# Kernel tuning notes

Hardware: AMD Instinct MI355X
Metric: run time of the kernel (lower is better)

The kernel has to match this reference:

```python
import jax, jax.numpy as jnp
import numpy as np
from jax import lax

B, CIN, H, W = 16, 64, 128, 128
NUM_CLASSES = 80
K = 100              # cfg.TEST.TOPK
SCORE_THRESH = 0.2   # hardcoded in decode()
NMS_THRESH = 0.5     # cfg.TEST.NMS_THRESH
RATIO = 4.0          # inp_downsample_ratio


def setup_inputs() -> dict:
    key = jax.random.key(0)
    ks = jax.random.split(key, 8)
    def w(k, shape, scale=0.05):
        return jax.random.normal(k, shape, dtype=jnp.float32) * scale
    inp = {"x": jax.random.normal(ks[0], (B, CIN, H, W), dtype=jnp.float32)}
    for i, (name, cout) in enumerate([("cls", NUM_CLASSES), ("reg", 2), ("wh", 2)]):
        inp[f"{name}_w1"] = w(ks[1 + 2 * i], (64, CIN, 3, 3))
        inp[f"{name}_b1"] = jnp.zeros((64,), jnp.float32)
        inp[f"{name}_w2"] = w(ks[2 + 2 * i], (cout, 64, 1, 1))
        # cls 1x1 conv bias filled with -2.19 as in the torch module
        inp[f"{name}_b2"] = jnp.full((cout,), -2.19 if name == "cls" else 0.0, jnp.float32)
    return inp


def _conv(x, w, b):
    y = lax.conv_general_dilated(x, w, (1, 1), 'SAME',
                                 dimension_numbers=('NCHW', 'OIHW', 'NCHW'))
    return y + b[None, :, None, None]


def _branch(x, w1, b1, w2, b2):
    return _conv(jax.nn.relu(_conv(x, w1, b1)), w2, b2)


def _nms_keep(boxes, valid):
    # boxes: [K,4] sorted by score desc (top_k output); valid: [K] bool
    x1, y1, x2, y2 = boxes[:, 0], boxes[:, 1], boxes[:, 2], boxes[:, 3]
    area = (x2 - x1) * (y2 - y1)
    iw = jnp.clip(jnp.minimum(x2[:, None], x2[None, :]) - jnp.maximum(x1[:, None], x1[None, :]), 0.0)
    ih = jnp.clip(jnp.minimum(y2[:, None], y2[None, :]) - jnp.maximum(y1[:, None], y1[None, :]), 0.0)
    inter = iw * ih
    iou = inter / (area[:, None] + area[None, :] - inter + 1e-9)  # [K,K]
    idx = jnp.arange(K)
    def step(keep, i):
        sup = (iou[i] > NMS_THRESH) & (idx > i) & keep[i]
        return keep & ~sup, None
    keep, _ = lax.scan(step, valid, idx)
    return keep


def reference(x, cls_w1, cls_b1, cls_w2, cls_b2,
              reg_w1, reg_b1, reg_w2, reg_b2,
              wh_w1, wh_b1, wh_w2, wh_b2):
    cls = jax.nn.sigmoid(_branch(x, cls_w1, cls_b1, cls_w2, cls_b2))  # [B,C,H,W]
    reg = jax.nn.sigmoid(_branch(x, reg_w1, reg_b1, reg_w2, reg_b2))  # [B,2,H,W]
    wh = jnp.exp(_branch(x, wh_w1, wh_b1, wh_w2, wh_b2))              # [B,2,H,W]

    # 3x3 max-pool peak NMS (torch max_pool2d pads with -inf; SAME matches k=3,s=1,p=1)
    pooled = lax.reduce_window(cls, -jnp.inf, lax.max, (1, 1, 3, 3), (1, 1, 1, 1), 'SAME')
    cls = cls * (pooled == cls).astype(cls.dtype)

    cls_f = cls.transpose(0, 2, 3, 1).reshape(B, H * W, NUM_CLASSES)
    reg_f = reg.transpose(0, 2, 3, 1).reshape(B, H * W, 2)
    wh_f = wh.transpose(0, 2, 3, 1).reshape(B, H * W, 2)

    scores_all = jnp.max(cls_f, axis=-1)              # [B,HW]
    cats_all = jnp.argmax(cls_f, axis=-1)             # [B,HW]
    scores, inds = lax.top_k(scores_all, K)           # [B,K], sorted desc
    valid = scores > SCORE_THRESH                     # fixed-size mask instead of dynamic filter

    cats = jnp.take_along_axis(cats_all, inds, axis=1)
    reg_k = jnp.take_along_axis(reg_f, inds[..., None], axis=1)   # [B,K,2]
    wh_k = jnp.take_along_axis(wh_f, inds[..., None], axis=1)     # [B,K,2]

    gy, gx = jnp.meshgrid(jnp.arange(H), jnp.arange(W), indexing='ij')
    grids = jnp.stack([gx, gy], axis=-1).reshape(-1, 2).astype(jnp.float32)  # [HW,2] (x,y)
    ct = grids[inds] + reg_k                                       # [B,K,2]
    boxes = jnp.concatenate([ct - wh_k / 2.0, ct + wh_k / 2.0], axis=-1) * RATIO  # [B,K,4]

    keep = jax.vmap(_nms_keep)(boxes, valid)          # [B,K] bool
    return boxes, cats, scores, keep
```

## Files before the change

### kernel.cpp

```cpp
#include <hip/hip_runtime.h>
#include <math.h>

#define BN 16
#define HWSZ 16384
#define NC 80
#define KK 100

typedef _Float16 f16;
typedef _Float16 f16x2 __attribute__((ext_vector_type(2)));
typedef _Float16 f16x4 __attribute__((ext_vector_type(4)));
typedef _Float16 f16x8 __attribute__((ext_vector_type(8)));
typedef float    f32x4 __attribute__((ext_vector_type(4)));
typedef unsigned int uint;
typedef unsigned long long u64;

#define WS_CLS   0
#define CLS_SZ   (BN*NC*HWSZ)
#define WS_REG   (WS_CLS + CLS_SZ)
#define REG_SZ   (BN*2*HWSZ)
#define WS_WH    (WS_REG + REG_SZ)
#define WH_SZ    (BN*2*HWSZ)
#define WS_SC    (WS_WH + WH_SZ)
#define SC_SZ    (BN*HWSZ)
#define WS_CAT   (WS_SC + SC_SZ)
#define CAT_SZ   (BN*HWSZ)
#define WS_W1H   (WS_CAT + CAT_SZ)
#define W1F      (110592/2)
#define WS_W1L   (WS_W1H + W1F)
#define WS_W2H   (WS_W1L + W1F)
#define W2F      (7168/2)
#define WS_W2L   (WS_W2H + W2F)
#define NREG     (BN*128*2*2)
#define WS_XTH   (WS_W2L + W2F)
#define XT_F     (NREG*2112/2)
#define WS_XTL   (WS_XTH + XT_F)
#define WS_ZR    (WS_XTL + XT_F)
#define ZR_F     1056
#define WS_SC1   (WS_ZR + ZR_F)
#define WS_CAT1  (WS_SC1 + SC_SZ)
#define WS_SC2   (WS_CAT1 + CAT_SZ)
#define WS_CAT2  (WS_SC2 + SC_SZ)
#define WS_SC3   (WS_CAT2 + CAT_SZ)
#define WS_CAT3  (WS_SC3 + SC_SZ)
#define WS_SC4   (WS_CAT3 + CAT_SZ)
#define WS_CAT4  (WS_SC4 + SC_SZ)
#define WS_SC5   (WS_CAT4 + CAT_SZ)
#define WS_CAT5  (WS_SC5 + SC_SZ)
#define WS_SC6   (WS_CAT5 + CAT_SZ)
#define WS_CAT6  (WS_SC6 + SC_SZ)
#define WS_SC7   (WS_CAT6 + CAT_SZ)
#define WS_CAT7  (WS_SC7 + SC_SZ)
#define WS_END8  (WS_CAT7 + CAT_SZ)

#define SCL_X   16.0f
#define SCL_W   256.0f
#define INV_ACC (1.0f/4096.0f)

#define GL2LDS(g, l) __builtin_amdgcn_global_load_lds( \
    (__attribute__((address_space(1))) unsigned int*)(unsigned long long)(const void*)(g), \
    (__attribute__((address_space(3))) unsigned int*)(unsigned int)(unsigned long long)(void*)(l), \
    16, 0, 0)

__global__ void k_prep(const float* __restrict__ cw1, const float* __restrict__ rw1,
                       const float* __restrict__ ww1, const float* __restrict__ cw2,
                       const float* __restrict__ rw2, const float* __restrict__ ww2,
                       f16* __restrict__ w1h, f16* __restrict__ w1l,
                       f16* __restrict__ w2h, f16* __restrict__ w2l,
                       float* __restrict__ zr) {
    int idx = blockIdx.x * 256 + threadIdx.x;
    if (idx < 3*9*64*64) {
        int ci = idx & 63, co = (idx >> 6) & 63;
        int s  = (idx >> 12) % 9, br = idx / 36864;
        const float* src = (br == 0) ? cw1 : (br == 1 ? rw1 : ww1);
        float v = src[(co*64 + ci)*9 + s] * SCL_W;
        f16 h = (f16)v;
        w1h[idx] = h; w1l[idx] = (f16)(v - (float)h);
    }
    int j = idx - 3*9*64*64;
    if (j >= 0 && j < 112*64) {
        int ci = j & 63, row = j >> 6;
        float v = 0.f;
        if (row < 80)                    v = cw2[row*64 + ci];
        else if (row < 82)               v = rw2[(row-80)*64 + ci];
        else if (row >= 96 && row < 98)  v = ww2[(row-96)*64 + ci];
        v *= SCL_W;
        f16 h = (f16)v;
        w2h[j] = h; w2l[j] = (f16)(v - (float)h);
    }
    if (zr && idx < ZR_F) zr[idx] = 0.f;
}

__global__ __launch_bounds__(256) void k_prepx(const float* __restrict__ x,
                                               f16* __restrict__ xth,
                                               f16* __restrict__ xtl) {
    const int reg = blockIdx.x;
    const int chunk = reg & 1, hh = (reg >> 1) & 1;
    const int gy = (reg >> 2) & 127, b = reg >> 9;
    __shared__ f16 th[66*72] __attribute__((aligned(16)));
    __shared__ f16 tl[66*72] __attribute__((aligned(16)));
    const int tid = threadIdx.x;
    const float* xb = x + ((size_t)(b*64 + chunk*32))*HWSZ + gy*128;
    #pragma unroll
    for (int it = 0; it < 9; it++) {
        int idx = it*256 + tid;
        if (idx < 2112) {
            int ci = idx / 66, pxi = idx - ci*66;
            int gp = hh*64 - 1 + pxi;
            float v = 0.f;
            if (gp >= 0 && gp < 128) v = xb[(size_t)ci*HWSZ + gp] * SCL_X;
            f16 hv = (f16)v;
            th[pxi*72 + ci] = hv;
            tl[pxi*72 + ci] = (f16)(v - (float)hv);
        }
    }
    __syncthreads();
    f16* oh = xth + (size_t)reg*2112;
    f16* ol = xtl + (size_t)reg*2112;
    {
        int row = tid >> 2, q = tid & 3;
        int sq = q ^ ((row >> 1) & 3);
        *(f16x8*)(oh + row*32 + sq*8) = *(const f16x8*)(th + row*72 + q*8);
        *(f16x8*)(ol + row*32 + sq*8) = *(const f16x8*)(tl + row*72 + q*8);
        if (tid < 8) {
            int u2 = 256 + tid, row2 = u2 >> 2, q2 = u2 & 3;
            int sq2 = q2 ^ ((row2 >> 1) & 3);
            *(f16x8*)(oh + row2*32 + sq2*8) = *(const f16x8*)(th + row2*72 + q2*8);
            *(f16x8*)(ol + row2*32 + sq2*8) = *(const f16x8*)(tl + row2*72 + q2*8);
        }
    }
}

#define ABUF 8448
__global__ __launch_bounds__(256, 2) void k_conv(
    const f16* __restrict__ xth, const f16* __restrict__ xtl, const f16* __restrict__ zreg,
    const f16* __restrict__ w1h, const f16* __restrict__ w1l,
    const f16* __restrict__ w2h, const f16* __restrict__ w2l,
    const float* __restrict__ b1c, const float* __restrict__ b1r, const float* __restrict__ b1w,
    const float* __restrict__ b2c, const float* __restrict__ b2r, const float* __restrict__ b2w,
    float* __restrict__ cls_o, float* __restrict__ reg_o, float* __restrict__ wh_o)
{
    __shared__ char smem[7*ABUF] __attribute__((aligned(16)));
    f16* Rh = (f16*)smem;
    f16* Rl = (f16*)(smem + 9216);

    const int p  = blockIdx.x + 2*blockIdx.y + 128*blockIdx.z;
    const int lg = (p & 7)*256 + (p >> 3);
    const int b  = lg >> 7;
    const int y0 = ((lg & 127) >> 1) * 2;
    const int h  = lg & 1;

    const int tid = threadIdx.x;
    const int w = tid >> 6, lane = tid & 63;
    const int l15 = lane & 15, quad = lane >> 4;
    const int co = w*16 + l15;

    #define STAGE1(ch, gyi, bufi) do {                                        \
        const int gy_ = y0 - 1 + (gyi);                                       \
        const f16* sh_; const f16* sl_;                                       \
        if (gy_ >= 0 && gy_ < 128) {                                          \
            size_t ro_ = (size_t)(((b*128 + gy_)*2 + h)*2 + (ch)) * 2112;     \
            sh_ = xth + ro_; sl_ = xtl + ro_;                                 \
        } else { sh_ = zreg; sl_ = zreg; }                                    \
        char* db_ = smem + (bufi)*ABUF;                                       \
        GL2LDS(sh_ + tid*8, db_ + tid*16);                                    \
        GL2LDS(sl_ + tid*8, db_ + 4224 + tid*16);                             \
        if (tid < 8) {                                                        \
            GL2LDS(sh_ + 2048 + tid*8, db_ + 4096 + tid*16);                  \
            GL2LDS(sl_ + 2048 + tid*8, db_ + 4224 + 4096 + tid*16);           \
        }                                                                     \
    } while (0)

    f32x4 accA[3][4], accB[3][4];
    #pragma unroll
    for (int br = 0; br < 3; br++)
        #pragma unroll
        for (int m = 0; m < 4; m++) {
            accA[br][m] = (f32x4){0.f,0.f,0.f,0.f};
            accB[br][m] = (f32x4){0.f,0.f,0.f,0.f};
        }

    #define CSTEP(ph, rr, A0p, A1p) do {                                      \
        const f16* A0 = (const f16*)(A0p);                                    \
        const f16* A1 = (const f16*)(A1p);                                    \
        _Pragma("unroll")                                                     \
        for (int dx = 0; dx < 3; dx++) {                                      \
            const int s = (rr)*3 + dx;                                        \
            f16x8 bh[3], bl[3];                                               \
            _Pragma("unroll")                                                 \
            for (int br = 0; br < 3; br++) {                                  \
                size_t k = ((size_t)((br*9 + s)*64 + co))*64 + (ph)*32 + quad*8; \
                bh[br] = *(const f16x8*)(w1h + k);                            \
                bl[br] = *(const f16x8*)(w1l + k);                            \
            }                                                                 \
            __builtin_amdgcn_s_setprio(1);                                    \
            _Pragma("unroll")                                                 \
            for (int m = 0; m < 4; m++) {                                     \
                const int row = m*16 + l15 + dx;                              \
                const int off = row*32 + ((quad ^ ((row >> 1) & 3)) << 3);    \
                {                                                             \
                    f16x8 ah0 = *(const f16x8*)(A0 + off);                    \
                    f16x8 al0 = *(const f16x8*)(A0 + 2112 + off);             \
                    _Pragma("unroll")                                         \
                    for (int br = 0; br < 3; br++) {                          \
                        accA[br][m] = __builtin_amdgcn_mfma_f32_16x16x32_f16(ah0, bh[br], accA[br][m], 0,0,0); \
                        accA[br][m] = __builtin_amdgcn_mfma_f32_16x16x32_f16(ah0, bl[br], accA[br][m], 0,0,0); \
                        accA[br][m] = __builtin_amdgcn_mfma_f32_16x16x32_f16(al0, bh[br], accA[br][m], 0,0,0); \
                    }                                                         \
                }                                                             \
                {                                                             \
                    f16x8 ah1 = *(const f16x8*)(A1 + off);                    \
                    f16x8 al1 = *(const f16x8*)(A1 + 2112 + off);             \
                    _Pragma("unroll")                                         \
                    for (int br = 0; br < 3; br++) {                          \
                        accB[br][m] = __builtin_amdgcn_mfma_f32_16x16x32_f16(ah1, bh[br], accB[br][m], 0,0,0); \
                        accB[br][m] = __builtin_amdgcn_mfma_f32_16x16x32_f16(ah1, bl[br], accB[br][m], 0,0,0); \
                        accB[br][m] = __builtin_amdgcn_mfma_f32_16x16x32_f16(al1, bh[br], accB[br][m], 0,0,0); \
                    }                                                         \
                }                                                             \
            }                                                                 \
            __builtin_amdgcn_s_setprio(0);                                    \
        }                                                                     \
    } while (0)

    #pragma unroll
    for (int gyi = 0; gyi < 4; gyi++) STAGE1(0, gyi, gyi);
    #pragma unroll
    for (int gyi = 0; gyi < 3; gyi++) STAGE1(1, gyi, 4 + gyi);
    __syncthreads();

    for (int r = 0; r < 3; r++)
        CSTEP(0, r, smem + r*ABUF, smem + (r+1)*ABUF);

    __syncthreads();
    STAGE1(1, 3, 0);

    for (int r = 0; r < 2; r++)
        CSTEP(1, r, smem + (4+r)*ABUF, smem + (5+r)*ABUF);

    __syncthreads();
    CSTEP(1, 2, smem + 6*ABUF, smem + 0*ABUF);

    #undef STAGE1
    #undef CSTEP

    #define EPIROW(ACC, yy) do {                                              \
        __syncthreads();                        \
        _Pragma("unroll")                                                     \
        for (int m = 0; m < 4; m++)                                           \
            _Pragma("unroll")                                                 \
            for (int rg = 0; rg < 4; rg++) {                                  \
                float t = fmaxf(ACC[br][m][rg]*INV_ACC + b1v, 0.f) * SCL_X;   \
                f16 hh = (f16)t;                                              \
                int pxl = m*16 + quad*4 + rg;                                 \
                Rh[pxl*72 + co] = hh;                                         \
                Rl[pxl*72 + co] = (f16)(t - (float)hh);                       \
            }                                                                 \
        __syncthreads();                                                      \
        const int NT     = (br == 0) ? 5 : 1;                                 \
        const int rowoff = (br == 0) ? 0 : (br == 1 ? 80 : 96);               \
        f32x4 a2[5];                                                          \
        _Pragma("unroll")                                                     \
        for (int n = 0; n < 5; n++) a2[n] = (f32x4){0.f,0.f,0.f,0.f};         \
        _Pragma("unroll")                                                     \
        for (int kc = 0; kc < 64; kc += 32) {                                 \
            int off = co*72 + kc + quad*8;                                    \
            f16x8 xh = *(const f16x8*)(Rh + off);                             \
            f16x8 xl = *(const f16x8*)(Rl + off);                             \
            _Pragma("unroll")                                                 \
            for (int n = 0; n < 5; n++) {                                     \
                if (n >= NT) break;                                           \
                const f16* g2h = w2h + (rowoff + n*16 + l15)*64 + kc + quad*8;\
                const f16* g2l = w2l + (rowoff + n*16 + l15)*64 + kc + quad*8;\
                f16x8 bh2 = *(const f16x8*)g2h;                               \
                f16x8 bl2 = *(const f16x8*)g2l;                               \
                a2[n] = __builtin_amdgcn_mfma_f32_16x16x32_f16(xh, bh2, a2[n], 0,0,0); \
                a2[n] = __builtin_amdgcn_mfma_f32_16x16x32_f16(xh, bl2, a2[n], 0,0,0); \
                a2[n] = __builtin_amdgcn_mfma_f32_16x16x32_f16(xl, bh2, a2[n], 0,0,0); \
            }                                                                 \
        }                                                                     \
        const int pxg = h*64 + w*16 + quad*4;                                 \
        if (br == 0) {                                                        \
            _Pragma("unroll")                                                 \
            for (int n = 0; n < 5; n++) {                                     \
                int co2 = n*16 + l15;                                         \
                float bb = b2c[co2];                                          \
                _Pragma("unroll")                                             \
                for (int rg = 0; rg < 4; rg++) {                              \
                    float sv = a2[n][rg]*INV_ACC + bb;                        \
                    cls_o[((size_t)(b*80 + co2)*128 + (yy))*128 + pxg + rg] = 1.f/(1.f + expf(-sv)); \
                }                                                             \
            }                                                                 \
        } else {                                                              \
            if (l15 < 2) {                                                    \
                const float* b2 = (br == 1) ? b2r : b2w;                      \
                float* outp     = (br == 1) ? reg_o : wh_o;                   \
                float bb = b2[l15];                                           \
                _Pragma("unroll")                                             \
                for (int rg = 0; rg < 4; rg++) {                              \
                    float sv = a2[0][rg]*INV_ACC + bb;                        \
                    float o  = (br == 1) ? (1.f/(1.f + expf(-sv))) : expf(sv);\
                    outp[((size_t)(b*2 + l15))*HWSZ + (yy)*128 + pxg + rg] = o; \
                }                                                             \
            }                                                                 \
        }                                                                     \
    } while (0)

    #pragma unroll
    for (int br = 0; br < 3; br++) {
        const float* b1 = (br == 0) ? b1c : (br == 1 ? b1r : b1w);
        const float b1v = b1[co];
        EPIROW(accA, y0);
        EPIROW(accB, y0 + 1);
    }
    #undef EPIROW
}

#define A_STRIDE 36
#define ABUF_FB  9504
__global__ __launch_bounds__(256) void k_conv_fb(
    const float* __restrict__ x,
    const f16* __restrict__ w1h, const f16* __restrict__ w1l,
    const f16* __restrict__ w2h, const f16* __restrict__ w2l,
    const float* __restrict__ b1c, const float* __restrict__ b1r, const float* __restrict__ b1w,
    const float* __restrict__ b2c, const float* __restrict__ b2r, const float* __restrict__ b2w,
    float* __restrict__ cls_o, float* __restrict__ reg_o, float* __restrict__ wh_o)
{
    __shared__ char smem[19008] __attribute__((aligned(16)));
    f16* Rh = (f16*)smem;
    f16* Rl = (f16*)(smem + 9216);

    const int h = blockIdx.x, y = blockIdx.y, b = blockIdx.z;
    const int tid = threadIdx.x;
    const int w = tid >> 6, lane = tid & 63;
    const int l15 = lane & 15, quad = lane >> 4;

    static const int CS[6] = {0,0,0,1,1,1};
    static const int RS[6] = {0,1,2,0,1,2};

    #define STAGEF(bufi, si_) do {                                            \
        const int gy = y - 1 + RS[si_];                                       \
        const bool ok = (gy >= 0) && (gy < 128);                              \
        const float* xp = x + ((size_t)(b*64 + CS[si_]*32)*128 + gy)*128;     \
        f16x2* dh = (f16x2*)(smem + (bufi)*ABUF_FB);                          \
        f16x2* dl = (f16x2*)(smem + (bufi)*ABUF_FB + 4752);                   \
        _Pragma("unroll")                                                     \
        for (int e0 = 0; e0 < 1024; e0 += 256) {                              \
            int e = e0 + tid;                                                 \
            int pxl = e & 63, cp = e >> 6;                                    \
            float v0 = 0.f, v1 = 0.f;                                         \
            if (ok) { int g = h*64 + pxl;                                     \
                      v0 = xp[(size_t)(2*cp)*HWSZ + g]*SCL_X;                 \
                      v1 = xp[(size_t)(2*cp+1)*HWSZ + g]*SCL_X; }             \
            f16 h0 = (f16)v0, h1 = (f16)v1;                                   \
            f16 l0 = (f16)(v0 - (float)h0), l1 = (f16)(v1 - (float)h1);       \
            int wi = (pxl + 1)*18 + cp;                                       \
            dh[wi] = (f16x2){h0, h1};                                         \
            dl[wi] = (f16x2){l0, l1};                                         \
        }                                                                     \
        if (tid < 32) {                                                       \
            int side = tid >> 4, cp = tid & 15;                               \
            bool valid = ok && (side ? (h == 0) : (h == 1));                  \
            int g = side ? 64 : 63;                                           \
            float v0 = 0.f, v1 = 0.f;                                         \
            if (valid) { v0 = xp[(size_t)(2*cp)*HWSZ + g]*SCL_X;              \
                         v1 = xp[(size_t)(2*cp+1)*HWSZ + g]*SCL_X; }          \
            f16 h0 = (f16)v0, h1 = (f16)v1;                                   \
            f16 l0 = (f16)(v0 - (float)h0), l1 = (f16)(v1 - (float)h1);       \
            int wi = (side ? 65 : 0)*18 + cp;                                 \
            dh[wi] = (f16x2){h0, h1};                                         \
            dl[wi] = (f16x2){l0, l1};                                         \
        }                                                                     \
    } while (0)

    f32x4 acc[3][4];
    #pragma unroll
    for (int br = 0; br < 3; br++)
        #pragma unroll
        for (int m = 0; m < 4; m++) acc[br][m] = (f32x4){0.f,0.f,0.f,0.f};

    STAGEF(0, 0);
    __syncthreads();

    for (int si = 0; si < 6; si++) {
        const int cur = si & 1;
        if (si < 5) STAGEF(cur ^ 1, si + 1);
        const f16* APh = (const f16*)(smem + cur*ABUF_FB);
        const f16* APl = APh + 2376;
        const int chunk = CS[si], r = RS[si];
        #pragma unroll
        for (int dx = 0; dx < 3; dx++) {
            const int s = r*3 + dx;
            f16x8 bh[3], bl[3];
            #pragma unroll
            for (int br = 0; br < 3; br++) {
                size_t k = ((size_t)((br*9 + s)*64 + (w*16 + l15)))*64 + chunk*32 + quad*8;
                bh[br] = *(const f16x8*)(w1h + k);
                bl[br] = *(const f16x8*)(w1l + k);
            }
            #pragma unroll
            for (int m = 0; m < 4; m++) {
                int off = (m*16 + l15 + dx)*A_STRIDE + quad*8;
                f16x4 h0 = *(const f16x4*)(APh + off);
                f16x4 h1 = *(const f16x4*)(APh + off + 4);
                f16x4 u0 = *(const f16x4*)(APl + off);
                f16x4 u1 = *(const f16x4*)(APl + off + 4);
                f16x8 ah = __builtin_shufflevector(h0, h1, 0,1,2,3,4,5,6,7);
                f16x8 al = __builtin_shufflevector(u0, u1, 0,1,2,3,4,5,6,7);
                #pragma unroll
                for (int br = 0; br < 3; br++) {
                    acc[br][m] = __builtin_amdgcn_mfma_f32_16x16x32_f16(ah, bh[br], acc[br][m], 0,0,0);
                    acc[br][m] = __builtin_amdgcn_mfma_f32_16x16x32_f16(ah, bl[br], acc[br][m], 0,0,0);
                    acc[br][m] = __builtin_amdgcn_mfma_f32_16x16x32_f16(al, bh[br], acc[br][m], 0,0,0);
                }
            }
        }
        __syncthreads();
    }
    #undef STAGEF

    #pragma unroll
    for (int br = 0; br < 3; br++) {
        const float* b1 = (br == 0) ? b1c : (br == 1 ? b1r : b1w);
        const float b1v = b1[w*16 + l15];
        __syncthreads();
        #pragma unroll
        for (int m = 0; m < 4; m++)
            #pragma unroll
            for (int rg = 0; rg < 4; rg++) {
                float t = fmaxf(acc[br][m][rg]*INV_ACC + b1v, 0.f) * SCL_X;
                f16 hh = (f16)t;
                int pxl = m*16 + quad*4 + rg;
                int co  = w*16 + l15;
                Rh[pxl*72 + co] = hh;
                Rl[pxl*72 + co] = (f16)(t - (float)hh);
            }
        __syncthreads();

        const int NT     = (br == 0) ? 5 : 1;
        const int rowoff = (br == 0) ? 0 : (br == 1 ? 80 : 96);
        f32x4 a2[5];
        #pragma unroll
        for (int n = 0; n < 5; n++) a2[n] = (f32x4){0.f,0.f,0.f,0.f};

        #pragma unroll
        for (int kc = 0; kc < 64; kc += 32) {
            int off = (w*16 + l15)*72 + kc + quad*8;
            f16x8 xh = *(const f16x8*)(Rh + off);
            f16x8 xl = *(const f16x8*)(Rl + off);
            #pragma unroll
            for (int n = 0; n < 5; n++) {
                if (n >= NT) break;
                const f16* g2h = w2h + (rowoff + n*16 + l15)*64 + kc + quad*8;
                const f16* g2l = w2l + (rowoff + n*16 + l15)*64 + kc + quad*8;
                f16x8 bh = *(const f16x8*)g2h;
                f16x8 bl = *(const f16x8*)g2l;
                a2[n] = __builtin_amdgcn_mfma_f32_16x16x32_f16(xh, bh, a2[n], 0,0,0);
                a2[n] = __builtin_amdgcn_mfma_f32_16x16x32_f16(xh, bl, a2[n], 0,0,0);
                a2[n] = __builtin_amdgcn_mfma_f32_16x16x32_f16(xl, bh, a2[n], 0,0,0);
            }
        }

        const int pxg = h*64 + w*16 + quad*4;
        if (br == 0) {
            #pragma unroll
            for (int n = 0; n < 5; n++) {
                int co2 = n*16 + l15;
                float bb = b2c[co2];
                #pragma unroll
                for (int rg = 0; rg < 4; rg++) {
                    float sv = a2[n][rg]*INV_ACC + bb;
                    cls_o[((size_t)(b*80 + co2)*128 + y)*128 + pxg + rg] = 1.f/(1.f + expf(-sv));
                }
            }
        } else {
            if (l15 < 2) {
                const float* b2 = (br == 1) ? b2r : b2w;
                float* outp     = (br == 1) ? reg_o : wh_o;
                float bb = b2[l15];
                #pragma unroll
                for (int rg = 0; rg < 4; rg++) {
                    float sv = a2[0][rg]*INV_ACC + bb;
                    float o  = (br == 1) ? (1.f/(1.f + expf(-sv))) : expf(sv);
                    outp[((size_t)(b*2 + l15))*HWSZ + y*128 + pxg + rg] = o;
                }
            }
        }
    }
}

__global__ __launch_bounds__(256) void k_peaks(const float* __restrict__ cls,
                                               float* __restrict__ s0, int* __restrict__ c0p,
                                               float* __restrict__ s1, int* __restrict__ c1p,
                                               float* __restrict__ s2, int* __restrict__ c2p,
                                               float* __restrict__ s3, int* __restrict__ c3p,
                                               float* __restrict__ s4, int* __restrict__ c4p,
                                               float* __restrict__ s5, int* __restrict__ c5p,
                                               float* __restrict__ s6, int* __restrict__ c6p,
                                               float* __restrict__ s7, int* __restrict__ c7p,
                                               int span) {
    const int b  = blockIdx.y;
    const int z  = blockIdx.z;
    const int c0 = z * span, c1 = c0 + span;
    float* __restrict__ sc  = (z == 0) ? s0 : (z == 1) ? s1 : (z == 2) ? s2 : (z == 3) ? s3
                            : (z == 4) ? s4 : (z == 5) ? s5 : (z == 6) ? s6 : s7;
    int*   __restrict__ cat = (z == 0) ? c0p : (z == 1) ? c1p : (z == 2) ? c2p : (z == 3) ? c3p
                            : (z == 4) ? c4p : (z == 5) ? c5p : (z == 6) ? c6p : c7p;
    const int wv = threadIdx.x >> 6;
    const int l  = threadIdx.x & 63;
    const int y0 = blockIdx.x * 16 + wv * 4;
    const int p0 = l * 2;
    const bool gt = (y0 > 0);
    const bool gb = (y0 + 4 < 128);
    float best[8]; int bc[8];
    #pragma unroll
    for (int i = 0; i < 8; i++) { best[i] = -1.f; bc[i] = c0; }
    for (int c = c0; c < c1; c++) {
        const float* pl = cls + (size_t)(b*80 + c)*HWSZ + y0*128 + p0;
        float2 t[6];
        t[0] = gt ? *(const float2*)(pl - 128) : make_float2(-1e30f, -1e30f);
        t[1] = *(const float2*)pl;
        t[2] = *(const float2*)(pl + 128);
        t[3] = *(const float2*)(pl + 256);
        t[4] = *(const float2*)(pl + 384);
        t[5] = gb ? *(const float2*)(pl + 512) : make_float2(-1e30f, -1e30f);
        #pragma unroll
        for (int i = 0; i < 4; i++) {
            float vm0 = fmaxf(t[i+1].x, fmaxf(t[i].x, t[i+2].x));
            float vm1 = fmaxf(t[i+1].y, fmaxf(t[i].y, t[i+2].y));
            float lft = __shfl_up(vm1, 1);   if (l == 0)  lft = -1e30f;
            float rgt = __shfl_down(vm0, 1); if (l == 63) rgt = -1e30f;
            float m0 = fmaxf(lft, fmaxf(vm0, vm1));
            float m1 = fmaxf(vm0, fmaxf(vm1, rgt));
            float k0 = (t[i+1].x == m0) ? t[i+1].x : 0.f;
            float k1 = (t[i+1].y == m1) ? t[i+1].y : 0.f;
            if (k0 > best[2*i])   { best[2*i]   = k0; bc[2*i]   = c; }
            if (k1 > best[2*i+1]) { best[2*i+1] = k1; bc[2*i+1] = c; }
        }
    }
    #pragma unroll
    for (int i = 0; i < 4; i++) {
        int o = b*HWSZ + (y0 + i)*128 + p0;
        *(float2*)&sc[o] = make_float2(best[2*i], best[2*i+1]);
        *(int2*)&cat[o]  = make_int2(bc[2*i], bc[2*i+1]);
    }
}

__global__ __launch_bounds__(256) void k_merge8(
        float* __restrict__ d0, int* __restrict__ e0,
        const float* __restrict__ s1, const int* __restrict__ c1,
        const float* __restrict__ s2, const int* __restrict__ c2,
        const float* __restrict__ s3, const int* __restrict__ c3,
        const float* __restrict__ s4, const int* __restrict__ c4,
        const float* __restrict__ s5, const int* __restrict__ c5,
        const float* __restrict__ s6, const int* __restrict__ c6,
        const float* __restrict__ s7, const int* __restrict__ c7) {
    int i = (blockIdx.x * 256 + threadIdx.x) * 4;
    float4 a = *(const float4*)(d0 + i);
    int4   ca = *(const int4*)(e0 + i);
    #define MRG(SS, CC) do {                                                  \
        float4 bq = *(const float4*)((SS) + i);                               \
        int4   cb = *(const int4*)((CC) + i);                                 \
        if (bq.x > a.x) { a.x = bq.x; ca.x = cb.x; }                          \
        if (bq.y > a.y) { a.y = bq.y; ca.y = cb.y; }                          \
        if (bq.z > a.z) { a.z = bq.z; ca.z = cb.z; }                          \
        if (bq.w > a.w) { a.w = bq.w; ca.w = cb.w; }                          \
    } while (0)
    MRG(s1, c1); MRG(s2, c2); MRG(s3, c3); MRG(s4, c4);
    MRG(s5, c5); MRG(s6, c6); MRG(s7, c7);
    #undef MRG
    *(float4*)(d0 + i) = a;
    *(int4*)(e0 + i)  = ca;
}

__global__ __launch_bounds__(256) void k_select(const float* __restrict__ sc,
                                                const int* __restrict__ cats,
                                                const float* __restrict__ regp,
                                                const float* __restrict__ whp,
                                                float* __restrict__ out) {
    const int b   = blockIdx.x;
    const int tid = threadIdx.x;
    const int wv  = tid >> 6, lane = tid & 63;
    const float* scb = sc + (size_t)b*HWSZ;

    __shared__ int   red[2][4];
    __shared__ uint  wtot[4];
    __shared__ int   gib[128];
    __shared__ uint  gvb[128];
    __shared__ int   ebuf[KK];
    __shared__ u64   keys[128];
    __shared__ int   s_inds[KK];
    __shared__ float s_vals[KK];
    __shared__ float X1[KK], Y1[KK], X2[KK], Y2[KK], AR[KK];

    f32x4 d[16];
    #pragma unroll
    for (int c = 0; c < 16; c++)
        d[c] = *(const f32x4*)(scb + c*1024 + tid*4);

    #define CNT_GT(T, OUTV) do {                                              \
        int myc_ = 0;                                                         \
        _Pragma("unroll")                                                     \
        for (int c = 0; c < 16; c++) {                                        \
            _Pragma("unroll")                                                 \
            for (int j = 0; j < 4; j++)                                       \
                myc_ += (__float_as_uint(d[c][j]) > (T)) ? 1 : 0;             \
        }                                                                     \
        _Pragma("unroll")                                                     \
        for (int o_ = 32; o_ >= 1; o_ >>= 1) myc_ += __shfl_xor(myc_, o_);    \
        if (lane == 0) red[par][wv] = myc_;                                   \
        __syncthreads();                                                      \
        OUTV = red[par][0] + red[par][1] + red[par][2] + red[par][3];         \
        par ^= 1;                                                             \
    } while (0)

    int par = 0;
    uint Vbits; uint G;
    {
        int tot0; CNT_GT(0u, tot0);
        if (tot0 < KK) { Vbits = 0u; G = (uint)tot0; }
        else {
            uint lo = 0u, hi = 0x7F800000u; int gHi = 0;
            while (hi - lo > 1u) {
                uint mid = lo + ((hi - lo) >> 1);
                int t_; CNT_GT(mid, t_);
                if (t_ >= KK) lo = mid; else { hi = mid; gHi = t_; }
            }
            Vbits = hi; G = (uint)gHi;
        }
    }
    #undef CNT_GT
    const uint Eneed = KK - G;

    f32x4 c4[16];
    #pragma unroll
    for (int c = 0; c < 16; c++)
        c4[c] = *(const f32x4*)(scb + tid*64 + c*4);

    uint cntG = 0, cntE = 0;
    #pragma unroll
    for (int c = 0; c < 16; c++)
        #pragma unroll
        for (int j = 0; j < 4; j++) {
            uint u = __float_as_uint(c4[c][j]);
            cntG += (u > Vbits) ? 1u : 0u;
            cntE += (u == Vbits) ? 1u : 0u;
        }
    uint pk = (cntE << 16) | cntG;
    uint v = pk;
    #pragma unroll
    for (int o = 1; o <= 32; o <<= 1) {
        uint ov = __shfl_up(v, o);
        if (lane >= o) v += ov;
    }
    if (lane == 63) wtot[wv] = v;
    __syncthreads();
    uint woff = 0;
    for (int i = 0; i < 4; i++) if (i < wv) woff += wtot[i];
    uint excl = v - pk + woff;
    uint pG = excl & 0xFFFFu, pE = excl >> 16;

    #pragma unroll
    for (int c = 0; c < 16; c++)
        #pragma unroll
        for (int j = 0; j < 4; j++) {
            uint u = __float_as_uint(c4[c][j]);
            int idx = tid*64 + c*4 + j;
            if (u > Vbits) { gib[pG] = idx; gvb[pG] = u; pG++; }
            else if (u == Vbits) { if (pE < Eneed) ebuf[pE] = idx; pE++; }
        }
    __syncthreads();

    if (tid < 128)
        keys[tid] = (tid < (int)G) ? (((u64)(~gvb[tid]) << 32) | (uint)gib[tid])
                                   : ~0ull;
    for (uint k2 = 2; k2 <= 128; k2 <<= 1) {
        for (uint j = k2 >> 1; j > 0; j >>= 1) {
            __syncthreads();
            if (tid < 128) {
                uint i = (uint)tid, ixj = i ^ j;
                if (ixj > i) {
                    u64 a = keys[i], bb = keys[ixj];
                    bool up = ((i & k2) == 0);
                    if ((a > bb) == up) { keys[i] = bb; keys[ixj] = a; }
                }
            }
        }
    }
    __syncthreads();

    if (tid < KK) {
        if (tid < (int)G) {
            u64 kk2 = keys[tid];
            s_inds[tid] = (int)(uint)kk2;
            s_vals[tid] = __uint_as_float(~(uint)(kk2 >> 32));
        } else {
            s_inds[tid] = ebuf[tid - (int)G];
            s_vals[tid] = __uint_as_float(Vbits);
        }
    }
    __syncthreads();

    if (tid < KK) {
        int ind   = s_inds[tid];
        float scv = s_vals[tid];
        const float* rb = regp + (size_t)b*2*HWSZ;
        const float* wb = whp  + (size_t)b*2*HWSZ;
        float r0 = rb[ind], r1 = rb[HWSZ + ind];
        float w0 = wb[ind], w1 = wb[HWSZ + ind];
        float ctx = (float)(ind & 127) + r0;
        float cty = (float)(ind >> 7) + r1;
        float x1 = (ctx - w0*0.5f)*4.f, y1 = (cty - w1*0.5f)*4.f;
        float x2 = (ctx + w0*0.5f)*4.f, y2 = (cty + w1*0.5f)*4.f;
        size_t bo = ((size_t)b*KK + tid)*4;
        out[bo+0] = x1; out[bo+1] = y1; out[bo+2] = x2; out[bo+3] = y2;
        out[BN*KK*4 + b*KK + tid]         = (float)cats[(size_t)b*HWSZ + ind];
        out[BN*KK*4 + BN*KK + b*KK + tid] = scv;
        X1[tid] = x1; Y1[tid] = y1; X2[tid] = x2; Y2[tid] = y2;
        AR[tid] = (x2 - x1)*(y2 - y1);
    }
    __syncthreads();

    if (tid < 64) {
        const int l = tid;
        float x1a = X1[l], y1a = Y1[l], x2a = X2[l], y2a = Y2[l], ara = AR[l];
        int   ka  = (s_vals[l] > 0.2f) ? 1 : 0;
        float x1b = 0, y1b = 0, x2b = 0, y2b = 0, arb = 0;
        int   kb  = 0;
        if (l < KK - 64) {
            x1b = X1[64+l]; y1b = Y1[64+l]; x2b = X2[64+l]; y2b = Y2[64+l];
            arb = AR[64+l];
            kb  = (s_vals[64+l] > 0.2f) ? 1 : 0;
        }
        for (int i = 0; i < KK; i++) {
            float jx1, jy1, jx2, jy2, jar; int jk;
            if (i < 64) {
                jx1 = __shfl(x1a, i); jy1 = __shfl(y1a, i);
                jx2 = __shfl(x2a, i); jy2 = __shfl(y2a, i);
                jar = __shfl(ara, i); jk  = __shfl(ka,  i);
            } else {
                int li = i - 64;
                jx1 = __shfl(x1b, li); jy1 = __shfl(y1b, li);
                jx2 = __shfl(x2b, li); jy2 = __shfl(y2b, li);
                jar = __shfl(arb, li); jk  = __shfl(kb,  li);
            }
            if (jk) {
                if (ka && l > i) {
                    float iw = fminf(jx2, x2a) - fmaxf(jx1, x1a); iw = iw > 0.f ? iw : 0.f;
                    float ih = fminf(jy2, y2a) - fmaxf(jy1, y1a); ih = ih > 0.f ? ih : 0.f;
                    float inter = iw*ih;
                    float iou = inter / (jar + ara - inter + 1e-9f);
                    if (iou > 0.5f) ka = 0;
                }
                if (kb && (64 + l) > i) {
                    float iw = fminf(jx2, x2b) - fmaxf(jx1, x1b); iw = iw > 0.f ? iw : 0.f;
                    float ih = fminf(jy2, y2b) - fmaxf(jy1, y1b); ih = ih > 0.f ? ih : 0.f;
                    float inter = iw*ih;
                    float iou = inter / (jar + arb - inter + 1e-9f);
                    if (iou > 0.5f) kb = 0;
                }
            }
        }
        int koff = BN*KK*4 + 2*BN*KK;
        out[koff + b*KK + l] = ka ? 1.f : 0.f;
        if (l < KK - 64) out[koff + b*KK + 64 + l] = kb ? 1.f : 0.f;
    }
}

extern "C" void kernel_launch(void* const* d_in, const int* in_sizes, int n_in,
                              void* d_out, int out_size, void* d_ws, size_t ws_size,
                              hipStream_t stream) {
    const float* x      = (const float*)d_in[0];
    const float* cls_w1 = (const float*)d_in[1];
    const float* cls_b1 = (const float*)d_in[2];
    const float* cls_w2 = (const float*)d_in[3];
    const float* cls_b2 = (const float*)d_in[4];
    const float* reg_w1 = (const float*)d_in[5];
    const float* reg_b1 = (const float*)d_in[6];
    const float* reg_w2 = (const float*)d_in[7];
    const float* reg_b2 = (const float*)d_in[8];
    const float* wh_w1  = (const float*)d_in[9];
    const float* wh_b1  = (const float*)d_in[10];
    const float* wh_w2  = (const float*)d_in[11];
    const float* wh_b2  = (const float*)d_in[12];

    float* ws   = (float*)d_ws;
    float* clsb = ws + WS_CLS;
    float* regb = ws + WS_REG;
    float* whb  = ws + WS_WH;
    float* scw  = ws + WS_SC;
    int*   cat  = (int*)(ws + WS_CAT);
    f16*   w1h  = (f16*)(ws + WS_W1H);
    f16*   w1l  = (f16*)(ws + WS_W1L);
    f16*   w2h  = (f16*)(ws + WS_W2H);
    f16*   w2l  = (f16*)(ws + WS_W2L);
    f16*   xth  = (f16*)(ws + WS_XTH);
    f16*   xtl  = (f16*)(ws + WS_XTL);
    f16*   zr   = (f16*)(ws + WS_ZR);
    float* out  = (float*)d_out;

    const bool big = ws_size >= (size_t)WS_END8 * 4u;

    k_prep<<<(3*9*64*64 + 112*64 + 255)/256, 256, 0, stream>>>(
        cls_w1, reg_w1, wh_w1, cls_w2, reg_w2, wh_w2, w1h, w1l, w2h, w2l,
        big ? (float*)(ws + WS_ZR) : (float*)0);
    if (big) {
        float* s1 = ws + WS_SC1;  int* c1 = (int*)(ws + WS_CAT1);
        float* s2 = ws + WS_SC2;  int* c2 = (int*)(ws + WS_CAT2);
        float* s3 = ws + WS_SC3;  int* c3 = (int*)(ws + WS_CAT3);
        float* s4 = ws + WS_SC4;  int* c4 = (int*)(ws + WS_CAT4);
        float* s5 = ws + WS_SC5;  int* c5 = (int*)(ws + WS_CAT5);
        float* s6 = ws + WS_SC6;  int* c6 = (int*)(ws + WS_CAT6);
        float* s7 = ws + WS_SC7;  int* c7 = (int*)(ws + WS_CAT7);
        k_prepx<<<NREG, 256, 0, stream>>>(x, xth, xtl);
        k_conv<<<dim3(2, 64, 16), 256, 0, stream>>>(
            xth, xtl, zr, w1h, w1l, w2h, w2l, cls_b1, reg_b1, wh_b1,
            cls_b2, reg_b2, wh_b2, clsb, regb, whb);
        k_peaks<<<dim3(8, 16, 8), 256, 0, stream>>>(
            clsb, scw, cat, s1, c1, s2, c2, s3, c3, s4, c4, s5, c5, s6, c6, s7, c7, 10);
        k_merge8<<<256, 256, 0, stream>>>(
            scw, cat, s1, c1, s2, c2, s3, c3, s4, c4, s5, c5, s6, c6, s7, c7);
    } else {
        k_conv_fb<<<dim3(2, 128, 16), 256, 0, stream>>>(
            x, w1h, w1l, w2h, w2l, cls_b1, reg_b1, wh_b1,
            cls_b2, reg_b2, wh_b2, clsb, regb, whb);
        k_peaks<<<dim3(8, 16, 1), 256, 0, stream>>>(
            clsb, scw, cat, scw, cat, scw, cat, scw, cat,
            scw, cat, scw, cat, scw, cat, scw, cat, 80);
    }
    k_select<<<16, 256, 0, stream>>>(scw, cat, regb, whb, out);
}
```

Measured before the change: 418.4 us.

## Merge per-chunk peak results with packed 64-bit atomicMax instead of merge kernel

Peak detection now packs score bits and inverted class index into a 64-bit key and combines the 8 class-chunk partial results through atomicMax into one zero-initialised buffer. This drops the k_merge8 kernel and the seven extra score/category planes it read. k_select reads the packed buffer and decodes the category from the low bits. Atomics add contention and the select pass now reads twice as many bytes per pixel. Inverting the class index in the low bits makes ties resolve to the lowest class, matching argmax.

```diff
diff --git a/kernel.cpp b/kernel.cpp
--- a/kernel.cpp
+++ b/kernel.cpp
@@ -30,27 +30,15 @@
 #define WS_W2H   (WS_W1L + W1F)
 #define W2F      (7168/2)
 #define WS_W2L   (WS_W2H + W2F)
+#define WS_PK    (WS_W2L + W2F)
+#define PK_F     (BN*HWSZ*2)
 #define NREG     (BN*128*2*2)
-#define WS_XTH   (WS_W2L + W2F)
+#define WS_XTH   (WS_PK + PK_F)
 #define XT_F     (NREG*2112/2)
 #define WS_XTL   (WS_XTH + XT_F)
 #define WS_ZR    (WS_XTL + XT_F)
 #define ZR_F     1056
-#define WS_SC1   (WS_ZR + ZR_F)
-#define WS_CAT1  (WS_SC1 + SC_SZ)
-#define WS_SC2   (WS_CAT1 + CAT_SZ)
-#define WS_CAT2  (WS_SC2 + SC_SZ)
-#define WS_SC3   (WS_CAT2 + CAT_SZ)
-#define WS_CAT3  (WS_SC3 + SC_SZ)
-#define WS_SC4   (WS_CAT3 + CAT_SZ)
-#define WS_CAT4  (WS_SC4 + SC_SZ)
-#define WS_SC5   (WS_CAT4 + CAT_SZ)
-#define WS_CAT5  (WS_SC5 + SC_SZ)
-#define WS_SC6   (WS_CAT5 + CAT_SZ)
-#define WS_CAT6  (WS_SC6 + SC_SZ)
-#define WS_SC7   (WS_CAT6 + CAT_SZ)
-#define WS_CAT7  (WS_SC7 + SC_SZ)
-#define WS_END8  (WS_CAT7 + CAT_SZ)
+#define WS_END   (WS_ZR + ZR_F)
 
 #define SCL_X   16.0f
 #define SCL_W   256.0f
@@ -66,7 +54,7 @@
                        const float* __restrict__ rw2, const float* __restrict__ ww2,
                        f16* __restrict__ w1h, f16* __restrict__ w1l,
                        f16* __restrict__ w2h, f16* __restrict__ w2l,
-                       float* __restrict__ zr) {
+                       float* __restrict__ zr, u64* __restrict__ pkz) {
     int idx = blockIdx.x * 256 + threadIdx.x;
     if (idx < 3*9*64*64) {
         int ci = idx & 63, co = (idx >> 6) & 63;
@@ -88,6 +76,10 @@
         w2h[j] = h; w2l[j] = (f16)(v - (float)h);
     }
     if (zr && idx < ZR_F) zr[idx] = 0.f;
+    if (idx < 32768) {
+        #pragma unroll
+        for (int q = 0; q < 8; q++) pkz[idx*8 + q] = 0ull;
+    }
 }
 
 __global__ __launch_bounds__(256) void k_prepx(const float* __restrict__ x,
@@ -489,22 +481,11 @@
 }
 
 __global__ __launch_bounds__(256) void k_peaks(const float* __restrict__ cls,
-                                               float* __restrict__ s0, int* __restrict__ c0p,
-                                               float* __restrict__ s1, int* __restrict__ c1p,
-                                               float* __restrict__ s2, int* __restrict__ c2p,
-                                               float* __restrict__ s3, int* __restrict__ c3p,
-                                               float* __restrict__ s4, int* __restrict__ c4p,
-                                               float* __restrict__ s5, int* __restrict__ c5p,
-                                               float* __restrict__ s6, int* __restrict__ c6p,
-                                               float* __restrict__ s7, int* __restrict__ c7p,
+                                               u64* __restrict__ pk,
                                                int span) {
     const int b  = blockIdx.y;
     const int z  = blockIdx.z;
     const int c0 = z * span, c1 = c0 + span;
-    float* __restrict__ sc  = (z == 0) ? s0 : (z == 1) ? s1 : (z == 2) ? s2 : (z == 3) ? s3
-                            : (z == 4) ? s4 : (z == 5) ? s5 : (z == 6) ? s6 : s7;
-    int*   __restrict__ cat = (z == 0) ? c0p : (z == 1) ? c1p : (z == 2) ? c2p : (z == 3) ? c3p
-                            : (z == 4) ? c4p : (z == 5) ? c5p : (z == 6) ? c6p : c7p;
     const int wv = threadIdx.x >> 6;
     const int l  = threadIdx.x & 63;
     const int y0 = blockIdx.x * 16 + wv * 4;
@@ -540,47 +521,21 @@
     #pragma unroll
     for (int i = 0; i < 4; i++) {
         int o = b*HWSZ + (y0 + i)*128 + p0;
-        *(float2*)&sc[o] = make_float2(best[2*i], best[2*i+1]);
-        *(int2*)&cat[o]  = make_int2(bc[2*i], bc[2*i+1]);
+        u64 k0 = ((u64)__float_as_uint(best[2*i])   << 32) | (uint)(79 - bc[2*i]);
+        u64 k1 = ((u64)__float_as_uint(best[2*i+1]) << 32) | (uint)(79 - bc[2*i+1]);
+        atomicMax((unsigned long long*)&pk[o],     (unsigned long long)k0);
+        atomicMax((unsigned long long*)&pk[o + 1], (unsigned long long)k1);
     }
 }
 
-__global__ __launch_bounds__(256) void k_merge8(
-        float* __restrict__ d0, int* __restrict__ e0,
-        const float* __restrict__ s1, const int* __restrict__ c1,
-        const float* __restrict__ s2, const int* __restrict__ c2,
-        const float* __restrict__ s3, const int* __restrict__ c3,
-        const float* __restrict__ s4, const int* __restrict__ c4,
-        const float* __restrict__ s5, const int* __restrict__ c5,
-        const float* __restrict__ s6, const int* __restrict__ c6,
-        const float* __restrict__ s7, const int* __restrict__ c7) {
-    int i = (blockIdx.x * 256 + threadIdx.x) * 4;
-    float4 a = *(const float4*)(d0 + i);
-    int4   ca = *(const int4*)(e0 + i);
-    #define MRG(SS, CC) do {                                                  \
-        float4 bq = *(const float4*)((SS) + i);                               \
-        int4   cb = *(const int4*)((CC) + i);                                 \
-        if (bq.x > a.x) { a.x = bq.x; ca.x = cb.x; }                          \
-        if (bq.y > a.y) { a.y = bq.y; ca.y = cb.y; }                          \
-        if (bq.z > a.z) { a.z = bq.z; ca.z = cb.z; }                          \
-        if (bq.w > a.w) { a.w = bq.w; ca.w = cb.w; }                          \
-    } while (0)
-    MRG(s1, c1); MRG(s2, c2); MRG(s3, c3); MRG(s4, c4);
-    MRG(s5, c5); MRG(s6, c6); MRG(s7, c7);
-    #undef MRG
-    *(float4*)(d0 + i) = a;
-    *(int4*)(e0 + i)  = ca;
-}
-
-__global__ __launch_bounds__(256) void k_select(const float* __restrict__ sc,
-                                                const int* __restrict__ cats,
+__global__ __launch_bounds__(256) void k_select(const u64* __restrict__ pk,
                                                 const float* __restrict__ regp,
                                                 const float* __restrict__ whp,
                                                 float* __restrict__ out) {
     const int b   = blockIdx.x;
     const int tid = threadIdx.x;
     const int wv  = tid >> 6, lane = tid & 63;
-    const float* scb = sc + (size_t)b*HWSZ;
+    const u64* pkb = pk + (size_t)b*HWSZ;
 
     __shared__ int   red[2][4];
     __shared__ uint  wtot[4];
@@ -592,19 +547,19 @@
     __shared__ float s_vals[KK];
     __shared__ float X1[KK], Y1[KK], X2[KK], Y2[KK], AR[KK];
 
-    f32x4 d[16];
-    #pragma unroll
-    for (int c = 0; c < 16; c++)
-        d[c] = *(const f32x4*)(scb + c*1024 + tid*4);
+    uint dd[64];
+    #pragma unroll
+    for (int c = 0; c < 32; c++) {
+        ulonglong2 q = *(const ulonglong2*)(pkb + c*512 + tid*2);
+        dd[2*c]   = (uint)(q.x >> 32);
+        dd[2*c+1] = (uint)(q.y >> 32);
+    }
 
     #define CNT_GT(T, OUTV) do {                                              \
         int myc_ = 0;                                                         \
         _Pragma("unroll")                                                     \
-        for (int c = 0; c < 16; c++) {                                        \
-            _Pragma("unroll")                                                 \
-            for (int j = 0; j < 4; j++)                                       \
-                myc_ += (__float_as_uint(d[c][j]) > (T)) ? 1 : 0;             \
-        }                                                                     \
+        for (int c = 0; c < 64; c++)                                          \
+            myc_ += (dd[c] > (T)) ? 1 : 0;                                    \
         _Pragma("unroll")                                                     \
         for (int o_ = 32; o_ >= 1; o_ >>= 1) myc_ += __shfl_xor(myc_, o_);    \
         if (lane == 0) red[par][wv] = myc_;                                   \
@@ -631,22 +586,22 @@
     #undef CNT_GT
     const uint Eneed = KK - G;
 
-    f32x4 c4[16];
-    #pragma unroll
-    for (int c = 0; c < 16; c++)
-        c4[c] = *(const f32x4*)(scb + tid*64 + c*4);
+    uint cc[64];
+    #pragma unroll
+    for (int c = 0; c < 32; c++) {
+        ulonglong2 q = *(const ulonglong2*)(pkb + tid*64 + c*2);
+        cc[2*c]   = (uint)(q.x >> 32);
+        cc[2*c+1] = (uint)(q.y >> 32);
+    }
 
     uint cntG = 0, cntE = 0;
     #pragma unroll
-    for (int c = 0; c < 16; c++)
-        #pragma unroll
-        for (int j = 0; j < 4; j++) {
-            uint u = __float_as_uint(c4[c][j]);
-            cntG += (u > Vbits) ? 1u : 0u;
-            cntE += (u == Vbits) ? 1u : 0u;
-        }
-    uint pk = (cntE << 16) | cntG;
-    uint v = pk;
+    for (int c = 0; c < 64; c++) {
+        cntG += (cc[c] > Vbits) ? 1u : 0u;
+        cntE += (cc[c] == Vbits) ? 1u : 0u;
+    }
+    uint pkd = (cntE << 16) | cntG;
+    uint v = pkd;
     #pragma unroll
     for (int o = 1; o <= 32; o <<= 1) {
         uint ov = __shfl_up(v, o);
@@ -656,18 +611,16 @@
     __syncthreads();
     uint woff = 0;
     for (int i = 0; i < 4; i++) if (i < wv) woff += wtot[i];
-    uint excl = v - pk + woff;
+    uint excl = v - pkd + woff;
     uint pG = excl & 0xFFFFu, pE = excl >> 16;
 
     #pragma unroll
-    for (int c = 0; c < 16; c++)
-        #pragma unroll
-        for (int j = 0; j < 4; j++) {
-            uint u = __float_as_uint(c4[c][j]);
-            int idx = tid*64 + c*4 + j;
-            if (u > Vbits) { gib[pG] = idx; gvb[pG] = u; pG++; }
-            else if (u == Vbits) { if (pE < Eneed) ebuf[pE] = idx; pE++; }
-        }
+    for (int c = 0; c < 64; c++) {
+        uint u = cc[c];
+        int idx = tid*64 + c;
+        if (u > Vbits) { gib[pG] = idx; gvb[pG] = u; pG++; }
+        else if (u == Vbits) { if (pE < Eneed) ebuf[pE] = idx; pE++; }
+    }
     __syncthreads();
 
     if (tid < 128)
@@ -703,6 +656,8 @@
     if (tid < KK) {
         int ind   = s_inds[tid];
         float scv = s_vals[tid];
+        u64 pv    = pkb[ind];
+        int catv  = 79 - (int)(uint)(pv & 0xFFFFFFFFull);
         const float* rb = regp + (size_t)b*2*HWSZ;
         const float* wb = whp  + (size_t)b*2*HWSZ;
         float r0 = rb[ind], r1 = rb[HWSZ + ind];
@@ -713,7 +668,7 @@
         float x2 = (ctx + w0*0.5f)*4.f, y2 = (cty + w1*0.5f)*4.f;
         size_t bo = ((size_t)b*KK + tid)*4;
         out[bo+0] = x1; out[bo+1] = y1; out[bo+2] = x2; out[bo+3] = y2;
-        out[BN*KK*4 + b*KK + tid]         = (float)cats[(size_t)b*HWSZ + ind];
+        out[BN*KK*4 + b*KK + tid]         = (float)catv;
         out[BN*KK*4 + BN*KK + b*KK + tid] = scv;
         X1[tid] = x1; Y1[tid] = y1; X2[tid] = x2; Y2[tid] = y2;
         AR[tid] = (x2 - x1)*(y2 - y1);
@@ -787,45 +742,32 @@
     float* clsb = ws + WS_CLS;
     float* regb = ws + WS_REG;
     float* whb  = ws + WS_WH;
-    float* scw  = ws + WS_SC;
-    int*   cat  = (int*)(ws + WS_CAT);
     f16*   w1h  = (f16*)(ws + WS_W1H);
     f16*   w1l  = (f16*)(ws + WS_W1L);
     f16*   w2h  = (f16*)(ws + WS_W2H);
     f16*   w2l  = (f16*)(ws + WS_W2L);
+    u64*   pkb  = (u64*)(ws + WS_PK);
     f16*   xth  = (f16*)(ws + WS_XTH);
     f16*   xtl  = (f16*)(ws + WS_XTL);
     f16*   zr   = (f16*)(ws + WS_ZR);
     float* out  = (float*)d_out;
 
-    const bool big = ws_size >= (size_t)WS_END8 * 4u;
+    const bool big = ws_size >= (size_t)WS_END * 4u;
 
     k_prep<<<(3*9*64*64 + 112*64 + 255)/256, 256, 0, stream>>>(
         cls_w1, reg_w1, wh_w1, cls_w2, reg_w2, wh_w2, w1h, w1l, w2h, w2l,
-        big ? (float*)(ws + WS_ZR) : (float*)0);
+        big ? (float*)(ws + WS_ZR) : (float*)0, pkb);
     if (big) {
-        float* s1 = ws + WS_SC1;  int* c1 = (int*)(ws + WS_CAT1);
-        float* s2 = ws + WS_SC2;  int* c2 = (int*)(ws + WS_CAT2);
-        float* s3 = ws + WS_SC3;  int* c3 = (int*)(ws + WS_CAT3);
-        float* s4 = ws + WS_SC4;  int* c4 = (int*)(ws + WS_CAT4);
-        float* s5 = ws + WS_SC5;  int* c5 = (int*)(ws + WS_CAT5);
-        float* s6 = ws + WS_SC6;  int* c6 = (int*)(ws + WS_CAT6);
-        float* s7 = ws + WS_SC7;  int* c7 = (int*)(ws + WS_CAT7);
         k_prepx<<<NREG, 256, 0, stream>>>(x, xth, xtl);
         k_conv<<<dim3(2, 64, 16), 256, 0, stream>>>(
             xth, xtl, zr, w1h, w1l, w2h, w2l, cls_b1, reg_b1, wh_b1,
             cls_b2, reg_b2, wh_b2, clsb, regb, whb);
-        k_peaks<<<dim3(8, 16, 8), 256, 0, stream>>>(
-            clsb, scw, cat, s1, c1, s2, c2, s3, c3, s4, c4, s5, c5, s6, c6, s7, c7, 10);
-        k_merge8<<<256, 256, 0, stream>>>(
-            scw, cat, s1, c1, s2, c2, s3, c3, s4, c4, s5, c5, s6, c6, s7, c7);
+        k_peaks<<<dim3(8, 16, 8), 256, 0, stream>>>(clsb, pkb, 10);
     } else {
         k_conv_fb<<<dim3(2, 128, 16), 256, 0, stream>>>(
             x, w1h, w1l, w2h, w2l, cls_b1, reg_b1, wh_b1,
             cls_b2, reg_b2, wh_b2, clsb, regb, whb);
-        k_peaks<<<dim3(8, 16, 1), 256, 0, stream>>>(
-            clsb, scw, cat, scw, cat, scw, cat, scw, cat,
-            scw, cat, scw, cat, scw, cat, scw, cat, 80);
-    }
-    k_select<<<16, 256, 0, stream>>>(scw, cat, regb, whb, out);
+        k_peaks<<<dim3(8, 16, 1), 256, 0, stream>>>(clsb, pkb, 80);
+    }
+    k_select<<<16, 256, 0, stream>>>(pkb, regb, whb, out);
 }
```

New measurement: 440.2 us. +5.2%, slower.
